# Performance work log

Hardware: AMD Instinct MI355X
Metric: run time of the kernel (lower is better)

## Reference

```python
import jax, jax.numpy as jnp
import numpy as np

H, W, C = 56, 56, 192
WS, SS = 7, 3          # window_size, shift_size
NH, HD = 6, 32         # num_heads, head_dim
N = WS * WS            # tokens per window = 49
HIDDEN = 4 * C
EPS = 1e-5


def _rel_pos_index():
    coords = np.stack(np.meshgrid(np.arange(WS), np.arange(WS), indexing='ij'))  # (2,ws,ws)
    flat = coords.reshape(2, -1)
    rel = flat[:, :, None] - flat[:, None, :]            # (2,N,N)
    rel = rel.transpose(1, 2, 0)
    rel[:, :, 0] += WS - 1
    rel[:, :, 1] += WS - 1
    rel[:, :, 0] *= 2 * WS - 1
    return rel.sum(-1)                                   # (N,N) int


def _attn_mask():
    img = np.zeros((H, W))
    cnt = 0
    for hs in (slice(0, -WS), slice(-WS, -SS), slice(-SS, None)):
        for ws_ in (slice(0, -WS), slice(-WS, -SS), slice(-SS, None)):
            img[hs, ws_] = cnt
            cnt += 1
    mw = img.reshape(H // WS, WS, W // WS, WS).transpose(0, 2, 1, 3).reshape(-1, N)  # (nW,N)
    diff = mw[:, None, :] - mw[:, :, None]
    return np.where(diff != 0, -100.0, 0.0).astype(np.float32)  # (nW,N,N)


REL_IDX = jnp.asarray(_rel_pos_index())
ATTN_MASK = jnp.asarray(_attn_mask())


def _ln(x, w, b):
    mu = x.mean(-1, keepdims=True)
    var = ((x - mu) ** 2).mean(-1, keepdims=True)
    return (x - mu) * jax.lax.rsqrt(var + EPS) * w + b


def _window_partition(x):
    # (B,H,W,C) -> (B*nW, N, C)
    B = x.shape[0]
    x = x.reshape(B, H // WS, WS, W // WS, WS, C)
    x = x.transpose(0, 1, 3, 2, 4, 5)
    return x.reshape(-1, N, C)


def _window_reverse(win, B):
    # (B*nW, N, C) -> (B,H,W,C)
    x = win.reshape(B, H // WS, W // WS, WS, WS, C)
    x = x.transpose(0, 1, 3, 2, 4, 5)
    return x.reshape(B, H, W, C)


def setup_inputs() -> dict:
    key = jax.random.key(0)
    ks = jax.random.split(key, 16)
    s = 0.02
    return {
        'x': jax.random.normal(ks[0], (64, H * W, C), jnp.float32),
        'norm1_w': jnp.ones((C,), jnp.float32),
        'norm1_b': jnp.zeros((C,), jnp.float32),
        'qkv_w': jax.random.normal(ks[1], (C, 3 * C), jnp.float32) * s,
        'qkv_b': jnp.zeros((3 * C,), jnp.float32),
        'rpb': jax.random.normal(ks[2], ((2 * WS - 1) ** 2, NH), jnp.float32) * s,
        'proj_w': jax.random.normal(ks[3], (C, C), jnp.float32) * s,
        'proj_b': jnp.zeros((C,), jnp.float32),
        'norm2_w': jnp.ones((C,), jnp.float32),
        'norm2_b': jnp.zeros((C,), jnp.float32),
        'fc1_w': jax.random.normal(ks[4], (C, HIDDEN), jnp.float32) * s,
        'fc1_b': jnp.zeros((HIDDEN,), jnp.float32),
        'fc2_w': jax.random.normal(ks[5], (HIDDEN, C), jnp.float32) * s,
        'fc2_b': jnp.zeros((C,), jnp.float32),
    }


def reference(x, norm1_w, norm1_b, qkv_w, qkv_b, rpb, proj_w, proj_b,
              norm2_w, norm2_b, fc1_w, fc1_b, fc2_w, fc2_b):
    B = x.shape[0]
    nW = (H // WS) * (W // WS)
    shortcut = x
    h = _ln(x, norm1_w, norm1_b).reshape(B, H, W, C)
    # cyclic shift
    h = jnp.roll(h, shift=(-SS, -SS), axis=(1, 2))
    xw = _window_partition(h)                                   # (B*nW, N, C)
    # windowed MHA
    qkv = (xw @ qkv_w + qkv_b).reshape(-1, N, 3, NH, HD).transpose(2, 0, 3, 1, 4)
    q, k, v = qkv[0], qkv[1], qkv[2]                            # (Bn, NH, N, HD)
    scale = HD ** -0.5
    attn = jnp.einsum('bhnd,bhmd->bhnm', q * scale, k)          # (Bn, NH, N, N)
    bias = rpb[REL_IDX.reshape(-1)].reshape(N, N, NH).transpose(2, 0, 1)
    attn = attn + bias[None]
    attn = attn.reshape(B, nW, NH, N, N) + ATTN_MASK[None, :, None]
    attn = jax.nn.softmax(attn.reshape(-1, NH, N, N), axis=-1)
    out = jnp.einsum('bhnm,bhmd->bhnd', attn, v)
    out = out.transpose(0, 2, 1, 3).reshape(-1, N, C)
    out = out @ proj_w + proj_b
    # reverse windows + un-shift
    h = _window_reverse(out, B)
    h = jnp.roll(h, shift=(SS, SS), axis=(1, 2)).reshape(B, H * W, C)
    x = shortcut + h
    # MLP (exact GELU, as torch nn.GELU default)
    m = _ln(x, norm2_w, norm2_b)
    m = jax.nn.gelu(m @ fc1_w + fc1_b, approximate=False)
    m = m @ fc2_w + fc2_b
    return x + m
```

## Files before the change

kernel.cpp:

```cpp
#include <hip/hip_runtime.h>
#include <hip/hip_bf16.h>

typedef __hip_bfloat16 bf16;
typedef __attribute__((ext_vector_type(8))) short short8;
typedef __attribute__((ext_vector_type(4))) float floatx4;

__device__ __forceinline__ floatx4 mfma16(short8 a, short8 b, floatx4 c) {
  return __builtin_amdgcn_mfma_f32_16x16x32_bf16(a, b, c, 0, 0, 0);
}

__device__ __forceinline__ float wave_sum(float v) {
#pragma unroll
  for (int off = 1; off < 64; off <<= 1) v += __shfl_xor(v, off);
  return v;
}

__device__ __forceinline__ void gload16(const void* g, void* l) {
  __builtin_amdgcn_global_load_lds(
      (const __attribute__((address_space(1))) unsigned int*)g,
      (__attribute__((address_space(3))) unsigned int*)l, 16, 0, 0);
}

__device__ __forceinline__ short8 lds_frag(const char* base, int row, int kb) {
  return *(const short8*)(base + row * 384 + (kb ^ ((row & 7) << 4)));
}
__device__ __forceinline__ short8 lds_frag128(const char* base, int row, int kb) {
  return *(const short8*)(base + row * 128 + (kb ^ ((row & 7) << 4)));
}

__global__ __launch_bounds__(256) void k_wt(const float* __restrict__ w,
                                            bf16* __restrict__ wt, int K, int N) {
  int id = blockIdx.x * 256 + threadIdx.x;
  if (id < K * N) {
    int n = id / K;
    int k = id - n * K;
    wt[id] = __float2bfloat16(w[(long)k * N + n]);
  }
}

template <bool GATHER>
__global__ __launch_bounds__(256) void k_ln(const float* __restrict__ xin,
                                            const float* __restrict__ w,
                                            const float* __restrict__ b,
                                            bf16* __restrict__ out) {
  const int lane = threadIdx.x & 63;
  const long row = (long)blockIdx.x * 4 + (threadIdx.x >> 6);
  long srow;
  if (GATHER) {
    int win = (int)(row / 49);
    int token = (int)(row - (long)win * 49);
    int bimg = win >> 6, wi = (win & 63) >> 3, wj = win & 7;
    int ti = token / 7, tj = token - ti * 7;
    int h = wi * 7 + ti + 3; if (h >= 56) h -= 56;
    int ww = wj * 7 + tj + 3; if (ww >= 56) ww -= 56;
    srow = (long)bimg * 3136 + h * 56 + ww;
  } else {
    srow = row;
  }
  const float* src = xin + srow * 192;
  float v0 = src[lane], v1 = src[lane + 64], v2 = src[lane + 128];
  float mu = wave_sum(v0 + v1 + v2) * (1.f / 192.f);
  float d0 = v0 - mu, d1 = v1 - mu, d2 = v2 - mu;
  float var = wave_sum(d0 * d0 + d1 * d1 + d2 * d2) * (1.f / 192.f);
  float rs = rsqrtf(var + 1e-5f);
  bf16* dst = out + row * 192;
  dst[lane]       = __float2bfloat16(d0 * rs * w[lane] + b[lane]);
  dst[lane + 64]  = __float2bfloat16(d1 * rs * w[lane + 64] + b[lane + 64]);
  dst[lane + 128] = __float2bfloat16(d2 * rs * w[lane + 128] + b[lane + 128]);
}

template <int EPI>
__global__ __launch_bounds__(256, 3) void k_gemm(const bf16* __restrict__ A,
                                                 const bf16* __restrict__ Bt,
                                                 const float* __restrict__ bias,
                                                 bf16* __restrict__ Cbf,
                                                 float* __restrict__ Cfp,
                                                 const float* __restrict__ res,
                                                 int Ncols, int K, long row0) {
  __shared__ __align__(16) char As[64 * 384];
  __shared__ __align__(16) char Bs[64 * 384];
  const int t = threadIdx.x;
  const int lane = t & 63, wid = t >> 6;
  const int lanelo = lane & 15, quad = lane >> 4;
  const long m0 = (long)blockIdx.x * 64;
  const int n0 = blockIdx.y * 64;
  const int wm = (wid >> 1) * 32, wn = (wid & 1) * 32;

  floatx4 acc[2][2];
#pragma unroll
  for (int i = 0; i < 2; i++)
#pragma unroll
    for (int j = 0; j < 2; j++) acc[i][j] = (floatx4){0.f, 0.f, 0.f, 0.f};

  const char* Ab = (const char*)(A + m0 * (long)K);
  const char* Bb = (const char*)(Bt + (long)n0 * K);
  const int ldab = 2 * K;

  for (int k0b = 0; k0b < 2 * K; k0b += 384) {
    __syncthreads();
#pragma unroll
    for (int i = 0; i < 6; i++) {
      int c = i * 256 + t;
      int r = c / 24;
      int j = c - r * 24;
      int be = (j * 16) ^ ((r & 7) << 4);
      gload16(Ab + (long)r * ldab + k0b + be, As + c * 16);
      gload16(Bb + (long)r * ldab + k0b + be, Bs + c * 16);
    }
    __syncthreads();

#pragma unroll
    for (int kk = 0; kk < 6; kk++) {
      const int kb = kk * 64 + quad * 16;
      short8 a0 = lds_frag(As, wm + lanelo, kb);
      short8 a1 = lds_frag(As, wm + 16 + lanelo, kb);
      short8 b0 = lds_frag(Bs, wn + lanelo, kb);
      short8 b1 = lds_frag(Bs, wn + 16 + lanelo, kb);
      acc[0][0] = mfma16(a0, b0, acc[0][0]);
      acc[0][1] = mfma16(a0, b1, acc[0][1]);
      acc[1][0] = mfma16(a1, b0, acc[1][0]);
      acc[1][1] = mfma16(a1, b1, acc[1][1]);
    }
  }

#pragma unroll
  for (int mi = 0; mi < 2; mi++) {
#pragma unroll
    for (int reg = 0; reg < 4; reg++) {
      const long r = m0 + wm + mi * 16 + quad * 4 + reg;
      long orow = r;
      if (EPI == 2) {
        const long rg = row0 + r;
        int win = (int)(rg / 49);
        int token = (int)(rg - (long)win * 49);
        int bimg = win >> 6, wi = (win & 63) >> 3, wj = win & 7;
        int ti = token / 7, tj = token - ti * 7;
        int h = wi * 7 + ti + 3; if (h >= 56) h -= 56;
        int ww = wj * 7 + tj + 3; if (ww >= 56) ww -= 56;
        orow = (long)bimg * 3136 + h * 56 + ww;
      }
#pragma unroll
      for (int ni = 0; ni < 2; ni++) {
        const int c = n0 + wn + ni * 16 + lanelo;
        float v = acc[mi][ni][reg] + bias[c];
        if (EPI == 0) {
          Cbf[r * Ncols + c] = __float2bfloat16(v);
        } else if (EPI == 1) {
          v = 0.5f * v * (1.f + erff(v * 0.70710678118654752f));
          Cbf[r * Ncols + c] = __float2bfloat16(v);
        } else if (EPI == 2) {
          Cfp[orow * 192 + c] = v + res[orow * 192 + c];
        } else {
          Cfp[r * 192 + c] = v + res[r * 192 + c];
        }
      }
    }
  }
}

__global__ __launch_bounds__(256, 3) void k_mlp(float* xres,
                                                const float* __restrict__ lw,
                                                const float* __restrict__ lb,
                                                const bf16* __restrict__ w1t,
                                                const float* __restrict__ b1,
                                                const bf16* __restrict__ w2t,
                                                const float* __restrict__ b2) {
  __shared__ __align__(16) char As[64 * 384];
  __shared__ __align__(16) char Hs[2][64 * 128];
  const int t = threadIdx.x, lane = t & 63, wid = t >> 6;
  const int lanelo = lane & 15, quad = lane >> 4;
  const long row0 = (long)blockIdx.x * 64;

  for (int i = 0; i < 16; i++) {
    int r = wid * 16 + i;
    const float* src = xres + (row0 + r) * 192;
    float v0 = src[lane], v1 = src[lane + 64], v2 = src[lane + 128];
    float mu = wave_sum(v0 + v1 + v2) * (1.f / 192.f);
    float d0 = v0 - mu, d1 = v1 - mu, d2 = v2 - mu;
    float var = wave_sum(d0 * d0 + d1 * d1 + d2 * d2) * (1.f / 192.f);
    float rs = rsqrtf(var + 1e-5f);
    int sw = (r & 7) << 4;
    *(bf16*)(As + r * 384 + ((2 * lane) ^ sw)) =
        __float2bfloat16(d0 * rs * lw[lane] + lb[lane]);
    *(bf16*)(As + r * 384 + ((128 + 2 * lane) ^ sw)) =
        __float2bfloat16(d1 * rs * lw[lane + 64] + lb[lane + 64]);
    *(bf16*)(As + r * 384 + ((256 + 2 * lane) ^ sw)) =
        __float2bfloat16(d2 * rs * lw[lane + 128] + lb[lane + 128]);
  }

  floatx4 acc2[4][3];
#pragma unroll
  for (int mi = 0; mi < 4; mi++)
#pragma unroll
    for (int ni = 0; ni < 3; ni++) acc2[mi][ni] = (floatx4){0.f, 0.f, 0.f, 0.f};

  __syncthreads();

  const int hcol = wid * 16 + lanelo;
  const int ocol0 = wid * 48;

  for (int nc = 0; nc < 12; nc++) {
    const char* w1p = (const char*)w1t + (long)(nc * 64 + hcol) * 384;
    floatx4 acc1[4];
#pragma unroll
    for (int mi = 0; mi < 4; mi++) acc1[mi] = (floatx4){0.f, 0.f, 0.f, 0.f};
#pragma unroll
    for (int kk = 0; kk < 6; kk++) {
      const int kb = kk * 64 + quad * 16;
      short8 bf = *(const short8*)(w1p + kb);
#pragma unroll
      for (int mi = 0; mi < 4; mi++) {
        short8 af = lds_frag(As, mi * 16 + lanelo, kb);
        acc1[mi] = mfma16(af, bf, acc1[mi]);
      }
    }

    char* H = Hs[nc & 1];
    const float b1v = b1[nc * 64 + hcol];
#pragma unroll
    for (int mi = 0; mi < 4; mi++)
#pragma unroll
      for (int reg = 0; reg < 4; reg++) {
        int r = mi * 16 + quad * 4 + reg;
        float v = acc1[mi][reg] + b1v;
        v = 0.5f * v * (1.f + erff(v * 0.70710678118654752f));
        *(bf16*)(H + r * 128 + ((2 * hcol) ^ ((r & 7) << 4))) =
            __float2bfloat16(v);
      }
    __syncthreads();

#pragma unroll
    for (int ks = 0; ks < 2; ks++) {
      const int kb = ks * 64 + quad * 16;
      short8 ha[4];
#pragma unroll
      for (int mi = 0; mi < 4; mi++)
        ha[mi] = lds_frag128(H, mi * 16 + lanelo, kb);
#pragma unroll
      for (int ni = 0; ni < 3; ni++) {
        short8 bv = *(const short8*)((const char*)w2t +
                                     (long)(ocol0 + ni * 16 + lanelo) * 1536 +
                                     nc * 128 + kb);
#pragma unroll
        for (int mi = 0; mi < 4; mi++)
          acc2[mi][ni] = mfma16(ha[mi], bv, acc2[mi][ni]);
      }
    }
  }

#pragma unroll
  for (int mi = 0; mi < 4; mi++)
#pragma unroll
    for (int ni = 0; ni < 3; ni++) {
      const int c = ocol0 + ni * 16 + lanelo;
      const float b2v = b2[c];
#pragma unroll
      for (int reg = 0; reg < 4; reg++) {
        const long g = (row0 + mi * 16 + quad * 4 + reg) * 192 + c;
        xres[g] = acc2[mi][ni][reg] + b2v + xres[g];
      }
    }
}

__global__ __launch_bounds__(256, 2) void k_attn(const bf16* __restrict__ qkv,
                                                 const float* __restrict__ rpb,
                                                 bf16* __restrict__ out) {
  __shared__ __align__(16) bf16 smem[4 * 7424];
  const int t = threadIdx.x, lane = t & 63, wid = t >> 6;
  const int lanelo = lane & 15, quad = lane >> 4;
  const int unit = blockIdx.x * 4 + wid;
  const int win = unit / 6, head = unit - win * 6;
  bf16* Qs = smem + wid * 7424;
  bf16* Ks = Qs + 2560;
  bf16* Vt = Qs + 5120;
  bf16* Ps = Qs;
  const long rowbase = (long)win * 49;
  const bf16* base = qkv + rowbase * 576 + head * 32;

  for (int idx = lane; idx < 196; idx += 64) {
    int tok = idx >> 2, ch = (idx & 3) * 8;
    *(uint4*)(&Qs[tok * 40 + ch]) = *(const uint4*)(base + (long)tok * 576 + ch);
    *(uint4*)(&Ks[tok * 40 + ch]) = *(const uint4*)(base + (long)tok * 576 + 192 + ch);
    union { uint4 u; bf16 h[8]; } tv;
    tv.u = *(const uint4*)(base + (long)tok * 576 + 384 + ch);
#pragma unroll
    for (int jj = 0; jj < 8; jj++) Vt[(ch + jj) * 72 + tok] = tv.h[jj];
  }
  for (int idx = lane; idx < 480; idx += 64) {
    int d = idx / 15, c = 49 + (idx - d * 15);
    Vt[d * 72 + c] = __float2bfloat16(0.f);
  }
  __syncthreads();

  floatx4 aS[4][4];
#pragma unroll
  for (int mi = 0; mi < 4; mi++)
#pragma unroll
    for (int ni = 0; ni < 4; ni++) aS[mi][ni] = (floatx4){0.f, 0.f, 0.f, 0.f};
  {
    short8 aq[4], bk[4];
#pragma unroll
    for (int mi = 0; mi < 4; mi++)
      aq[mi] = *(const short8*)(&Qs[(mi * 16 + lanelo) * 40 + quad * 8]);
#pragma unroll
    for (int ni = 0; ni < 4; ni++)
      bk[ni] = *(const short8*)(&Ks[(ni * 16 + lanelo) * 40 + quad * 8]);
#pragma unroll
    for (int mi = 0; mi < 4; mi++)
#pragma unroll
      for (int ni = 0; ni < 4; ni++) aS[mi][ni] = mfma16(aq[mi], bk[ni], aS[mi][ni]);
  }

  const int w_in = win & 63, wiw = w_in >> 3, wjw = w_in & 7;
  int cTi[4], cTj[4], cLab[4];
  bool cval[4];
#pragma unroll
  for (int ni = 0; ni < 4; ni++) {
    int j = ni * 16 + lanelo;
    cval[ni] = (j < 49);
    if (j > 48) j = 48;
    int ti = j / 7, tj = j - ti * 7;
    int rr = wiw * 7 + ti, cc = wjw * 7 + tj;
    cTi[ni] = ti;
    cTj[ni] = tj;
    cLab[ni] = ((rr < 49) ? 0 : (rr < 53 ? 1 : 2)) * 3 +
               ((cc < 49) ? 0 : (cc < 53 ? 1 : 2));
  }

  const float scale = 0.17677669529663687f;
  float rinv[16];
#pragma unroll
  for (int mi = 0; mi < 4; mi++) {
#pragma unroll
    for (int reg = 0; reg < 4; reg++) {
      int i = mi * 16 + quad * 4 + reg;
      if (i > 48) i = 48;
      int ti = i / 7, tj = i - ti * 7;
      int rr = wiw * 7 + ti, cc = wjw * 7 + tj;
      int rlab = ((rr < 49) ? 0 : (rr < 53 ? 1 : 2)) * 3 +
                 ((cc < 49) ? 0 : (cc < 53 ? 1 : 2));
      float sv[4];
      float mx = -1e30f;
#pragma unroll
      for (int ni = 0; ni < 4; ni++) {
        float s;
        if (cval[ni]) {
          int ridx = (ti - cTi[ni] + 6) * 13 + (tj - cTj[ni] + 6);
          float bb = rpb[ridx * 6 + head];
          if (rlab != cLab[ni]) bb -= 100.f;
          s = aS[mi][ni][reg] * scale + bb;
        } else {
          s = -1e30f;
        }
        sv[ni] = s;
        mx = fmaxf(mx, s);
      }
      mx = fmaxf(mx, __shfl_xor(mx, 1));
      mx = fmaxf(mx, __shfl_xor(mx, 2));
      mx = fmaxf(mx, __shfl_xor(mx, 4));
      mx = fmaxf(mx, __shfl_xor(mx, 8));
      float sum = 0.f;
#pragma unroll
      for (int ni = 0; ni < 4; ni++) {
        float p = __expf(sv[ni] - mx);
        sv[ni] = p;
        sum += p;
      }
      sum += __shfl_xor(sum, 1);
      sum += __shfl_xor(sum, 2);
      sum += __shfl_xor(sum, 4);
      sum += __shfl_xor(sum, 8);
      rinv[mi * 4 + reg] = 1.f / sum;
#pragma unroll
      for (int ni = 0; ni < 4; ni++) aS[mi][ni][reg] = sv[ni];
    }
  }
  __syncthreads();

#pragma unroll
  for (int mi = 0; mi < 4; mi++)
#pragma unroll
    for (int ni = 0; ni < 4; ni++)
#pragma unroll
      for (int reg = 0; reg < 4; reg++) {
        int i = mi * 16 + quad * 4 + reg, j = ni * 16 + lanelo;
        Ps[i * 72 + j] = __float2bfloat16(aS[mi][ni][reg]);
      }
  __syncthreads();

  floatx4 aO[4][2];
#pragma unroll
  for (int mi = 0; mi < 4; mi++)
#pragma unroll
    for (int ni = 0; ni < 2; ni++) aO[mi][ni] = (floatx4){0.f, 0.f, 0.f, 0.f};
#pragma unroll
  for (int k0 = 0; k0 < 64; k0 += 32) {
    short8 ap[4], bv[2];
#pragma unroll
    for (int mi = 0; mi < 4; mi++)
      ap[mi] = *(const short8*)(&Ps[(mi * 16 + lanelo) * 72 + k0 + quad * 8]);
#pragma unroll
    for (int ni = 0; ni < 2; ni++)
      bv[ni] = *(const short8*)(&Vt[(ni * 16 + lanelo) * 72 + k0 + quad * 8]);
#pragma unroll
    for (int mi = 0; mi < 4; mi++)
#pragma unroll
      for (int ni = 0; ni < 2; ni++) aO[mi][ni] = mfma16(ap[mi], bv[ni], aO[mi][ni]);
  }

#pragma unroll
  for (int mi = 0; mi < 4; mi++)
#pragma unroll
    for (int reg = 0; reg < 4; reg++) {
      int i = mi * 16 + quad * 4 + reg;
      if (i < 49) {
        float rv = rinv[mi * 4 + reg];
#pragma unroll
        for (int ni = 0; ni < 2; ni++) {
          int d = ni * 16 + lanelo;
          out[(rowbase + i) * 192 + head * 32 + d] =
              __float2bfloat16(aO[mi][ni][reg] * rv);
        }
      }
    }
}

extern "C" void kernel_launch(void* const* d_in, const int* in_sizes, int n_in,
                              void* d_out, int out_size, void* d_ws, size_t ws_size,
                              hipStream_t stream) {
  const float* x     = (const float*)d_in[0];
  const float* n1w   = (const float*)d_in[1];
  const float* n1b   = (const float*)d_in[2];
  const float* qkvw  = (const float*)d_in[3];
  const float* qkvb  = (const float*)d_in[4];
  const float* rpb   = (const float*)d_in[5];
  const float* projw = (const float*)d_in[6];
  const float* projb = (const float*)d_in[7];
  const float* n2w   = (const float*)d_in[8];
  const float* n2b   = (const float*)d_in[9];
  const float* fc1w  = (const float*)d_in[10];
  const float* fc1b  = (const float*)d_in[11];
  const float* fc2w  = (const float*)d_in[12];
  const float* fc2b  = (const float*)d_in[13];
  float* outf = (float*)d_out;

  const long CR = 50176;
  const int  NCH = 4;

  char* ws = (char*)d_ws;
  bf16* xw      = (bf16*)(ws + 0);
  bf16* qkvC    = (bf16*)(ws + 77070336LL);
  bf16* attC    = (bf16*)(ws + 134873088LL);
  bf16* wt_qkv  = (bf16*)(ws + 154140672LL);
  bf16* wt_proj = (bf16*)(ws + 154140672LL + 221184LL);
  bf16* wt_fc1  = (bf16*)(ws + 154140672LL + 294912LL);
  bf16* wt_fc2  = (bf16*)(ws + 154140672LL + 589824LL);

  k_wt<<<dim3((192 * 576 + 255) / 256), 256, 0, stream>>>(qkvw, wt_qkv, 192, 576);
  k_wt<<<dim3((192 * 192 + 255) / 256), 256, 0, stream>>>(projw, wt_proj, 192, 192);
  k_wt<<<dim3((192 * 768 + 255) / 256), 256, 0, stream>>>(fc1w, wt_fc1, 192, 768);
  k_wt<<<dim3((768 * 192 + 255) / 256), 256, 0, stream>>>(fc2w, wt_fc2, 768, 192);

  k_ln<true><<<dim3(50176), 256, 0, stream>>>(x, n1w, n1b, xw);

  for (int c = 0; c < NCH; c++) {
    const long r0 = c * CR;
    k_gemm<0><<<dim3(784, 9), 256, 0, stream>>>(xw + r0 * 192, wt_qkv, qkvb,
                                                qkvC, nullptr, nullptr, 576, 192, 0);
    k_attn<<<dim3(1536), 256, 0, stream>>>(qkvC, rpb, attC);
    k_gemm<2><<<dim3(784, 3), 256, 0, stream>>>(attC, wt_proj, projb, nullptr,
                                                outf, x, 192, 192, r0);
  }

  k_mlp<<<dim3(3136), 256, 0, stream>>>(outf, n2w, n2b, wt_fc1, fc1b,
                                        wt_fc2, fc2b);
}
```

Baseline: 1.020 ms.

## Fuse QKV GEMM, window attention and projection into one per-window kernel

```diff
diff --git a/kernel.cpp b/kernel.cpp
--- a/kernel.cpp
+++ b/kernel.cpp
@@ -3,6 +3,7 @@
 
 typedef __hip_bfloat16 bf16;
 typedef __attribute__((ext_vector_type(8))) short short8;
+typedef __attribute__((ext_vector_type(4))) short short4v;
 typedef __attribute__((ext_vector_type(4))) float floatx4;
 
 __device__ __forceinline__ floatx4 mfma16(short8 a, short8 b, floatx4 c) {
@@ -13,12 +14,6 @@
 #pragma unroll
   for (int off = 1; off < 64; off <<= 1) v += __shfl_xor(v, off);
   return v;
-}
-
-__device__ __forceinline__ void gload16(const void* g, void* l) {
-  __builtin_amdgcn_global_load_lds(
-      (const __attribute__((address_space(1))) unsigned int*)g,
-      (__attribute__((address_space(3))) unsigned int*)l, 16, 0, 0);
 }
 
 __device__ __forceinline__ short8 lds_frag(const char* base, int row, int kb) {
@@ -69,96 +64,219 @@
   dst[lane + 128] = __float2bfloat16(d2 * rs * w[lane + 128] + b[lane + 128]);
 }
 
-template <int EPI>
-__global__ __launch_bounds__(256, 3) void k_gemm(const bf16* __restrict__ A,
-                                                 const bf16* __restrict__ Bt,
-                                                 const float* __restrict__ bias,
-                                                 bf16* __restrict__ Cbf,
-                                                 float* __restrict__ Cfp,
-                                                 const float* __restrict__ res,
-                                                 int Ncols, int K, long row0) {
+__global__ __launch_bounds__(256, 2) void k_swin(const bf16* __restrict__ xw,
+                                                 const bf16* __restrict__ wq,
+                                                 const float* __restrict__ qkvb,
+                                                 const float* __restrict__ rpb,
+                                                 const bf16* __restrict__ wp,
+                                                 const float* __restrict__ projb,
+                                                 const float* __restrict__ xres,
+                                                 float* __restrict__ outf) {
   __shared__ __align__(16) char As[64 * 384];
-  __shared__ __align__(16) char Bs[64 * 384];
-  const int t = threadIdx.x;
-  const int lane = t & 63, wid = t >> 6;
+  __shared__ __align__(16) char Os[64 * 384];
+  __shared__ __align__(16) bf16 Qs[64 * 40];
+  __shared__ __align__(16) bf16 Ks[64 * 40];
+  __shared__ __align__(16) bf16 Vt[32 * 72];
+  __shared__ __align__(16) bf16 Ps[64 * 72];
+  const int t = threadIdx.x, lane = t & 63, wid = t >> 6;
   const int lanelo = lane & 15, quad = lane >> 4;
-  const long m0 = (long)blockIdx.x * 64;
-  const int n0 = blockIdx.y * 64;
-  const int wm = (wid >> 1) * 32, wn = (wid & 1) * 32;
-
-  floatx4 acc[2][2];
-#pragma unroll
-  for (int i = 0; i < 2; i++)
-#pragma unroll
-    for (int j = 0; j < 2; j++) acc[i][j] = (floatx4){0.f, 0.f, 0.f, 0.f};
-
-  const char* Ab = (const char*)(A + m0 * (long)K);
-  const char* Bb = (const char*)(Bt + (long)n0 * K);
-  const int ldab = 2 * K;
-
-  for (int k0b = 0; k0b < 2 * K; k0b += 384) {
-    __syncthreads();
+  const int w = blockIdx.x;
+  const long rowbase = (long)w * 49;
+  const int wm = wid * 16;
+
+  {
+    const char* src = (const char*)(xw + rowbase * 192);
 #pragma unroll
     for (int i = 0; i < 6; i++) {
       int c = i * 256 + t;
-      int r = c / 24;
-      int j = c - r * 24;
-      int be = (j * 16) ^ ((r & 7) << 4);
-      gload16(Ab + (long)r * ldab + k0b + be, As + c * 16);
-      gload16(Bb + (long)r * ldab + k0b + be, Bs + c * 16);
-    }
-    __syncthreads();
-
+      int r = c / 24, j = c - r * 24;
+      uint4 v;
+      if (r < 49) v = *(const uint4*)(src + (long)r * 384 + j * 16);
+      else { v.x = 0u; v.y = 0u; v.z = 0u; v.w = 0u; }
+      *(uint4*)(As + r * 384 + ((j * 16) ^ ((r & 7) << 4))) = v;
+    }
+  }
+
+  const int w_in = w & 63, wiw = w_in >> 3, wjw = w_in & 7;
+  int cTi[4], cTj[4], cLab[4];
+  bool cval[4];
+#pragma unroll
+  for (int ni = 0; ni < 4; ni++) {
+    int j = ni * 16 + lanelo;
+    cval[ni] = (j < 49);
+    if (j > 48) j = 48;
+    int ti = j / 7, tj = j - ti * 7;
+    int rr = wiw * 7 + ti, cc = wjw * 7 + tj;
+    cTi[ni] = ti; cTj[ni] = tj;
+    cLab[ni] = ((rr < 49) ? 0 : (rr < 53 ? 1 : 2)) * 3 +
+               ((cc < 49) ? 0 : (cc < 53 ? 1 : 2));
+  }
+  int ridx6[4][4];
+  float msub[4][4];
+#pragma unroll
+  for (int reg = 0; reg < 4; reg++) {
+    int i = wm + quad * 4 + reg;
+    if (i > 48) i = 48;
+    int ti = i / 7, tj = i - ti * 7;
+    int rr = wiw * 7 + ti, cc = wjw * 7 + tj;
+    int rlab = ((rr < 49) ? 0 : (rr < 53 ? 1 : 2)) * 3 +
+               ((cc < 49) ? 0 : (cc < 53 ? 1 : 2));
+#pragma unroll
+    for (int ni = 0; ni < 4; ni++) {
+      ridx6[reg][ni] = ((ti - cTi[ni] + 6) * 13 + (tj - cTj[ni] + 6)) * 6;
+      msub[reg][ni] = (rlab != cLab[ni]) ? 100.f : 0.f;
+    }
+  }
+  __syncthreads();
+
+  const float scale = 0.17677669529663687f;
+
+  for (int h = 0; h < 6; h++) {
+    floatx4 aq[6];
+#pragma unroll
+    for (int ni = 0; ni < 6; ni++) aq[ni] = (floatx4){0.f, 0.f, 0.f, 0.f};
 #pragma unroll
     for (int kk = 0; kk < 6; kk++) {
       const int kb = kk * 64 + quad * 16;
-      short8 a0 = lds_frag(As, wm + lanelo, kb);
-      short8 a1 = lds_frag(As, wm + 16 + lanelo, kb);
-      short8 b0 = lds_frag(Bs, wn + lanelo, kb);
-      short8 b1 = lds_frag(Bs, wn + 16 + lanelo, kb);
-      acc[0][0] = mfma16(a0, b0, acc[0][0]);
-      acc[0][1] = mfma16(a0, b1, acc[0][1]);
-      acc[1][0] = mfma16(a1, b0, acc[1][0]);
-      acc[1][1] = mfma16(a1, b1, acc[1][1]);
-    }
-  }
-
-#pragma unroll
-  for (int mi = 0; mi < 2; mi++) {
+      short8 af = lds_frag(As, wm + lanelo, kb);
+#pragma unroll
+      for (int ni = 0; ni < 6; ni++) {
+        const int wrow = (ni >> 1) * 192 + h * 32 + (ni & 1) * 16 + lanelo;
+        short8 bf = *(const short8*)((const char*)wq + (long)wrow * 384 + kb);
+        aq[ni] = mfma16(af, bf, aq[ni]);
+      }
+    }
+    __syncthreads();
+
+#pragma unroll
+    for (int ni = 0; ni < 6; ni++) {
+      const int p = ni >> 1;
+      const int d = (ni & 1) * 16 + lanelo;
+      const float bb = qkvb[p * 192 + h * 32 + d];
+      if (p < 2) {
+        bf16* dst = (p == 0) ? Qs : Ks;
+#pragma unroll
+        for (int reg = 0; reg < 4; reg++) {
+          int tok = wm + quad * 4 + reg;
+          dst[tok * 40 + d] = __float2bfloat16(aq[ni][reg] + bb);
+        }
+      } else {
+        union { short4v s; bf16 hh[4]; } pv;
+#pragma unroll
+        for (int reg = 0; reg < 4; reg++)
+          pv.hh[reg] = __float2bfloat16(aq[ni][reg] + bb);
+        *(short4v*)(&Vt[d * 72 + wm + quad * 4]) = pv.s;
+      }
+    }
+    __syncthreads();
+
+    short8 aqf = *(const short8*)(&Qs[(wm + lanelo) * 40 + quad * 8]);
+    floatx4 aS[4];
+#pragma unroll
+    for (int ni = 0; ni < 4; ni++) {
+      short8 bk = *(const short8*)(&Ks[(ni * 16 + lanelo) * 40 + quad * 8]);
+      aS[ni] = mfma16(aqf, bk, (floatx4){0.f, 0.f, 0.f, 0.f});
+    }
+
+    float rinv[4];
 #pragma unroll
     for (int reg = 0; reg < 4; reg++) {
-      const long r = m0 + wm + mi * 16 + quad * 4 + reg;
-      long orow = r;
-      if (EPI == 2) {
-        const long rg = row0 + r;
-        int win = (int)(rg / 49);
-        int token = (int)(rg - (long)win * 49);
-        int bimg = win >> 6, wi = (win & 63) >> 3, wj = win & 7;
-        int ti = token / 7, tj = token - ti * 7;
-        int h = wi * 7 + ti + 3; if (h >= 56) h -= 56;
-        int ww = wj * 7 + tj + 3; if (ww >= 56) ww -= 56;
-        orow = (long)bimg * 3136 + h * 56 + ww;
-      }
+      float sv[4];
+      float mx = -1e30f;
+#pragma unroll
+      for (int ni = 0; ni < 4; ni++) {
+        float s;
+        if (cval[ni]) {
+          s = aS[ni][reg] * scale + rpb[ridx6[reg][ni] + h] - msub[reg][ni];
+        } else {
+          s = -1e30f;
+        }
+        sv[ni] = s;
+        mx = fmaxf(mx, s);
+      }
+      mx = fmaxf(mx, __shfl_xor(mx, 1));
+      mx = fmaxf(mx, __shfl_xor(mx, 2));
+      mx = fmaxf(mx, __shfl_xor(mx, 4));
+      mx = fmaxf(mx, __shfl_xor(mx, 8));
+      float sum = 0.f;
+#pragma unroll
+      for (int ni = 0; ni < 4; ni++) {
+        float p = __expf(sv[ni] - mx);
+        sv[ni] = p;
+        sum += p;
+      }
+      sum += __shfl_xor(sum, 1);
+      sum += __shfl_xor(sum, 2);
+      sum += __shfl_xor(sum, 4);
+      sum += __shfl_xor(sum, 8);
+      rinv[reg] = 1.f / sum;
+#pragma unroll
+      for (int ni = 0; ni < 4; ni++) aS[ni][reg] = sv[ni];
+    }
+
+#pragma unroll
+    for (int ni = 0; ni < 4; ni++)
+#pragma unroll
+      for (int reg = 0; reg < 4; reg++)
+        Ps[(wm + quad * 4 + reg) * 72 + ni * 16 + lanelo] =
+            __float2bfloat16(aS[ni][reg]);
+
+    floatx4 aO[2];
+    aO[0] = (floatx4){0.f, 0.f, 0.f, 0.f};
+    aO[1] = (floatx4){0.f, 0.f, 0.f, 0.f};
+#pragma unroll
+    for (int ks = 0; ks < 2; ks++) {
+      short8 ap = *(const short8*)(&Ps[(wm + lanelo) * 72 + ks * 32 + quad * 8]);
 #pragma unroll
       for (int ni = 0; ni < 2; ni++) {
-        const int c = n0 + wn + ni * 16 + lanelo;
-        float v = acc[mi][ni][reg] + bias[c];
-        if (EPI == 0) {
-          Cbf[r * Ncols + c] = __float2bfloat16(v);
-        } else if (EPI == 1) {
-          v = 0.5f * v * (1.f + erff(v * 0.70710678118654752f));
-          Cbf[r * Ncols + c] = __float2bfloat16(v);
-        } else if (EPI == 2) {
-          Cfp[orow * 192 + c] = v + res[orow * 192 + c];
-        } else {
-          Cfp[r * 192 + c] = v + res[r * 192 + c];
-        }
-      }
-    }
-  }
-}
-
-__global__ __launch_bounds__(256, 3) void k_mlp(float* xres,
+        short8 bv = *(const short8*)(&Vt[(ni * 16 + lanelo) * 72 + ks * 32 + quad * 8]);
+        aO[ni] = mfma16(ap, bv, aO[ni]);
+      }
+    }
+#pragma unroll
+    for (int ni = 0; ni < 2; ni++)
+#pragma unroll
+      for (int reg = 0; reg < 4; reg++) {
+        int tok = wm + quad * 4 + reg;
+        int cb = 2 * (h * 32 + ni * 16 + lanelo);
+        *(bf16*)(Os + tok * 384 + (cb ^ ((tok & 7) << 4))) =
+            __float2bfloat16(aO[ni][reg] * rinv[reg]);
+      }
+  }
+  __syncthreads();
+
+  floatx4 accp[12];
+#pragma unroll
+  for (int ni = 0; ni < 12; ni++) accp[ni] = (floatx4){0.f, 0.f, 0.f, 0.f};
+#pragma unroll
+  for (int kk = 0; kk < 6; kk++) {
+    const int kb = kk * 64 + quad * 16;
+    short8 af = lds_frag(Os, wm + lanelo, kb);
+#pragma unroll
+    for (int ni = 0; ni < 12; ni++) {
+      short8 bf = *(const short8*)((const char*)wp +
+                                   (long)(ni * 16 + lanelo) * 384 + kb);
+      accp[ni] = mfma16(af, bf, accp[ni]);
+    }
+  }
+#pragma unroll
+  for (int reg = 0; reg < 4; reg++) {
+    const int tok = wm + quad * 4 + reg;
+    if (tok < 49) {
+      int ti = tok / 7, tj = tok - ti * 7;
+      int hh = wiw * 7 + ti + 3; if (hh >= 56) hh -= 56;
+      int ww2 = wjw * 7 + tj + 3; if (ww2 >= 56) ww2 -= 56;
+      const long orow = (long)(w >> 6) * 3136 + hh * 56 + ww2;
+#pragma unroll
+      for (int ni = 0; ni < 12; ni++) {
+        const int c = ni * 16 + lanelo;
+        outf[orow * 192 + c] = accp[ni][reg] + projb[c] + xres[orow * 192 + c];
+      }
+    }
+  }
+}
+
+__global__ __launch_bounds__(256, 4) void k_mlp(float* xres,
                                                 const float* __restrict__ lw,
                                                 const float* __restrict__ lb,
                                                 const bf16* __restrict__ w1t,
@@ -258,169 +376,6 @@
       for (int reg = 0; reg < 4; reg++) {
         const long g = (row0 + mi * 16 + quad * 4 + reg) * 192 + c;
         xres[g] = acc2[mi][ni][reg] + b2v + xres[g];
-      }
-    }
-}
-
-__global__ __launch_bounds__(256, 2) void k_attn(const bf16* __restrict__ qkv,
-                                                 const float* __restrict__ rpb,
-                                                 bf16* __restrict__ out) {
-  __shared__ __align__(16) bf16 smem[4 * 7424];
-  const int t = threadIdx.x, lane = t & 63, wid = t >> 6;
-  const int lanelo = lane & 15, quad = lane >> 4;
-  const int unit = blockIdx.x * 4 + wid;
-  const int win = unit / 6, head = unit - win * 6;
-  bf16* Qs = smem + wid * 7424;
-  bf16* Ks = Qs + 2560;
-  bf16* Vt = Qs + 5120;
-  bf16* Ps = Qs;
-  const long rowbase = (long)win * 49;
-  const bf16* base = qkv + rowbase * 576 + head * 32;
-
-  for (int idx = lane; idx < 196; idx += 64) {
-    int tok = idx >> 2, ch = (idx & 3) * 8;
-    *(uint4*)(&Qs[tok * 40 + ch]) = *(const uint4*)(base + (long)tok * 576 + ch);
-    *(uint4*)(&Ks[tok * 40 + ch]) = *(const uint4*)(base + (long)tok * 576 + 192 + ch);
-    union { uint4 u; bf16 h[8]; } tv;
-    tv.u = *(const uint4*)(base + (long)tok * 576 + 384 + ch);
-#pragma unroll
-    for (int jj = 0; jj < 8; jj++) Vt[(ch + jj) * 72 + tok] = tv.h[jj];
-  }
-  for (int idx = lane; idx < 480; idx += 64) {
-    int d = idx / 15, c = 49 + (idx - d * 15);
-    Vt[d * 72 + c] = __float2bfloat16(0.f);
-  }
-  __syncthreads();
-
-  floatx4 aS[4][4];
-#pragma unroll
-  for (int mi = 0; mi < 4; mi++)
-#pragma unroll
-    for (int ni = 0; ni < 4; ni++) aS[mi][ni] = (floatx4){0.f, 0.f, 0.f, 0.f};
-  {
-    short8 aq[4], bk[4];
-#pragma unroll
-    for (int mi = 0; mi < 4; mi++)
-      aq[mi] = *(const short8*)(&Qs[(mi * 16 + lanelo) * 40 + quad * 8]);
-#pragma unroll
-    for (int ni = 0; ni < 4; ni++)
-      bk[ni] = *(const short8*)(&Ks[(ni * 16 + lanelo) * 40 + quad * 8]);
-#pragma unroll
-    for (int mi = 0; mi < 4; mi++)
-#pragma unroll
-      for (int ni = 0; ni < 4; ni++) aS[mi][ni] = mfma16(aq[mi], bk[ni], aS[mi][ni]);
-  }
-
-  const int w_in = win & 63, wiw = w_in >> 3, wjw = w_in & 7;
-  int cTi[4], cTj[4], cLab[4];
-  bool cval[4];
-#pragma unroll
-  for (int ni = 0; ni < 4; ni++) {
-    int j = ni * 16 + lanelo;
-    cval[ni] = (j < 49);
-    if (j > 48) j = 48;
-    int ti = j / 7, tj = j - ti * 7;
-    int rr = wiw * 7 + ti, cc = wjw * 7 + tj;
-    cTi[ni] = ti;
-    cTj[ni] = tj;
-    cLab[ni] = ((rr < 49) ? 0 : (rr < 53 ? 1 : 2)) * 3 +
-               ((cc < 49) ? 0 : (cc < 53 ? 1 : 2));
-  }
-
-  const float scale = 0.17677669529663687f;
-  float rinv[16];
-#pragma unroll
-  for (int mi = 0; mi < 4; mi++) {
-#pragma unroll
-    for (int reg = 0; reg < 4; reg++) {
-      int i = mi * 16 + quad * 4 + reg;
-      if (i > 48) i = 48;
-      int ti = i / 7, tj = i - ti * 7;
-      int rr = wiw * 7 + ti, cc = wjw * 7 + tj;
-      int rlab = ((rr < 49) ? 0 : (rr < 53 ? 1 : 2)) * 3 +
-                 ((cc < 49) ? 0 : (cc < 53 ? 1 : 2));
-      float sv[4];
-      float mx = -1e30f;
-#pragma unroll
-      for (int ni = 0; ni < 4; ni++) {
-        float s;
-        if (cval[ni]) {
-          int ridx = (ti - cTi[ni] + 6) * 13 + (tj - cTj[ni] + 6);
-          float bb = rpb[ridx * 6 + head];
-          if (rlab != cLab[ni]) bb -= 100.f;
-          s = aS[mi][ni][reg] * scale + bb;
-        } else {
-          s = -1e30f;
-        }
-        sv[ni] = s;
-        mx = fmaxf(mx, s);
-      }
-      mx = fmaxf(mx, __shfl_xor(mx, 1));
-      mx = fmaxf(mx, __shfl_xor(mx, 2));
-      mx = fmaxf(mx, __shfl_xor(mx, 4));
-      mx = fmaxf(mx, __shfl_xor(mx, 8));
-      float sum = 0.f;
-#pragma unroll
-      for (int ni = 0; ni < 4; ni++) {
-        float p = __expf(sv[ni] - mx);
-        sv[ni] = p;
-        sum += p;
-      }
-      sum += __shfl_xor(sum, 1);
-      sum += __shfl_xor(sum, 2);
-      sum += __shfl_xor(sum, 4);
-      sum += __shfl_xor(sum, 8);
-      rinv[mi * 4 + reg] = 1.f / sum;
-#pragma unroll
-      for (int ni = 0; ni < 4; ni++) aS[mi][ni][reg] = sv[ni];
-    }
-  }
-  __syncthreads();
-
-#pragma unroll
-  for (int mi = 0; mi < 4; mi++)
-#pragma unroll
-    for (int ni = 0; ni < 4; ni++)
-#pragma unroll
-      for (int reg = 0; reg < 4; reg++) {
-        int i = mi * 16 + quad * 4 + reg, j = ni * 16 + lanelo;
-        Ps[i * 72 + j] = __float2bfloat16(aS[mi][ni][reg]);
-      }
-  __syncthreads();
-
-  floatx4 aO[4][2];
-#pragma unroll
-  for (int mi = 0; mi < 4; mi++)
-#pragma unroll
-    for (int ni = 0; ni < 2; ni++) aO[mi][ni] = (floatx4){0.f, 0.f, 0.f, 0.f};
-#pragma unroll
-  for (int k0 = 0; k0 < 64; k0 += 32) {
-    short8 ap[4], bv[2];
-#pragma unroll
-    for (int mi = 0; mi < 4; mi++)
-      ap[mi] = *(const short8*)(&Ps[(mi * 16 + lanelo) * 72 + k0 + quad * 8]);
-#pragma unroll
-    for (int ni = 0; ni < 2; ni++)
-      bv[ni] = *(const short8*)(&Vt[(ni * 16 + lanelo) * 72 + k0 + quad * 8]);
-#pragma unroll
-    for (int mi = 0; mi < 4; mi++)
-#pragma unroll
-      for (int ni = 0; ni < 2; ni++) aO[mi][ni] = mfma16(ap[mi], bv[ni], aO[mi][ni]);
-  }
-
-#pragma unroll
-  for (int mi = 0; mi < 4; mi++)
-#pragma unroll
-    for (int reg = 0; reg < 4; reg++) {
-      int i = mi * 16 + quad * 4 + reg;
-      if (i < 49) {
-        float rv = rinv[mi * 4 + reg];
-#pragma unroll
-        for (int ni = 0; ni < 2; ni++) {
-          int d = ni * 16 + lanelo;
-          out[(rowbase + i) * 192 + head * 32 + d] =
-              __float2bfloat16(aO[mi][ni][reg] * rv);
-        }
       }
     }
 }
@@ -444,13 +399,8 @@
   const float* fc2b  = (const float*)d_in[13];
   float* outf = (float*)d_out;
 
-  const long CR = 50176;
-  const int  NCH = 4;
-
   char* ws = (char*)d_ws;
   bf16* xw      = (bf16*)(ws + 0);
-  bf16* qkvC    = (bf16*)(ws + 77070336LL);
-  bf16* attC    = (bf16*)(ws + 134873088LL);
   bf16* wt_qkv  = (bf16*)(ws + 154140672LL);
   bf16* wt_proj = (bf16*)(ws + 154140672LL + 221184LL);
   bf16* wt_fc1  = (bf16*)(ws + 154140672LL + 294912LL);
@@ -463,14 +413,8 @@
 
   k_ln<true><<<dim3(50176), 256, 0, stream>>>(x, n1w, n1b, xw);
 
-  for (int c = 0; c < NCH; c++) {
-    const long r0 = c * CR;
-    k_gemm<0><<<dim3(784, 9), 256, 0, stream>>>(xw + r0 * 192, wt_qkv, qkvb,
-                                                qkvC, nullptr, nullptr, 576, 192, 0);
-    k_attn<<<dim3(1536), 256, 0, stream>>>(qkvC, rpb, attC);
-    k_gemm<2><<<dim3(784, 3), 256, 0, stream>>>(attC, wt_proj, projb, nullptr,
-                                                outf, x, 192, 192, r0);
-  }
+  k_swin<<<dim3(4096), 256, 0, stream>>>(xw, wt_qkv, qkvb, rpb, wt_proj, projb,
+                                         x, outf);
 
   k_mlp<<<dim3(3136), 256, 0, stream>>>(outf, n2w, n2b, wt_fc1, fc1b,
                                         wt_fc2, fc2b);
```

Measured after the change: 1.262 ms. 23.7% more time.

## Fuse QKV projection into windowed attention kernel and drop chunked launches

Applied to the files above, without the earlier changes.

```diff
diff --git a/kernel.cpp b/kernel.cpp
--- a/kernel.cpp
+++ b/kernel.cpp
@@ -3,6 +3,7 @@
 
 typedef __hip_bfloat16 bf16;
 typedef __attribute__((ext_vector_type(8))) short short8;
+typedef __attribute__((ext_vector_type(4))) short short4v;
 typedef __attribute__((ext_vector_type(4))) float floatx4;
 
 __device__ __forceinline__ floatx4 mfma16(short8 a, short8 b, floatx4 c) {
@@ -158,7 +159,192 @@
   }
 }
 
-__global__ __launch_bounds__(256, 3) void k_mlp(float* xres,
+__global__ __launch_bounds__(256, 2) void k_attn2(const bf16* __restrict__ xw,
+                                                  const bf16* __restrict__ wq,
+                                                  const float* __restrict__ qkvb,
+                                                  const float* __restrict__ rpb,
+                                                  bf16* __restrict__ attC) {
+  __shared__ __align__(16) bf16 smem[4 * 7424];
+  const int t = threadIdx.x, lane = t & 63, wid = t >> 6;
+  const int lanelo = lane & 15, quad = lane >> 4;
+  const int unit = blockIdx.x * 4 + wid;
+  const int win = unit / 6, head = unit - win * 6;
+  bf16* Qs = smem + wid * 7424;
+  bf16* Ks = Qs + 2560;
+  bf16* Vt = Qs + 5120;
+  bf16* Ps = Qs;
+  const long rowbase = (long)win * 49;
+
+  const int w_in = win & 63, wiw = w_in >> 3, wjw = w_in & 7;
+  int cTi[4], cTj[4], cLab[4];
+  bool cval[4];
+#pragma unroll
+  for (int ni = 0; ni < 4; ni++) {
+    int j = ni * 16 + lanelo;
+    cval[ni] = (j < 49);
+    if (j > 48) j = 48;
+    int ti = j / 7, tj = j - ti * 7;
+    int rr = wiw * 7 + ti, cc = wjw * 7 + tj;
+    cTi[ni] = ti; cTj[ni] = tj;
+    cLab[ni] = ((rr < 49) ? 0 : (rr < 53 ? 1 : 2)) * 3 +
+               ((cc < 49) ? 0 : (cc < 53 ? 1 : 2));
+  }
+
+  const float scale = 0.17677669529663687f;
+
+  {
+    floatx4 aq[4][6];
+#pragma unroll
+    for (int mi = 0; mi < 4; mi++)
+#pragma unroll
+      for (int ni = 0; ni < 6; ni++) aq[mi][ni] = (floatx4){0.f, 0.f, 0.f, 0.f};
+#pragma unroll
+    for (int kk = 0; kk < 6; kk++) {
+      const int kb = kk * 64 + quad * 16;
+      short8 af[4];
+#pragma unroll
+      for (int mi = 0; mi < 4; mi++)
+        af[mi] = *(const short8*)((const char*)xw +
+                                  (rowbase + mi * 16 + lanelo) * 384 + kb);
+#pragma unroll
+      for (int ni = 0; ni < 6; ni++) {
+        const int wrow = (ni >> 1) * 192 + head * 32 + (ni & 1) * 16 + lanelo;
+        short8 bf = *(const short8*)((const char*)wq + (long)wrow * 384 + kb);
+#pragma unroll
+        for (int mi = 0; mi < 4; mi++) aq[mi][ni] = mfma16(af[mi], bf, aq[mi][ni]);
+      }
+    }
+#pragma unroll
+    for (int ni = 0; ni < 6; ni++) {
+      const int p = ni >> 1;
+      const int d = (ni & 1) * 16 + lanelo;
+      const float bb = qkvb[p * 192 + head * 32 + d];
+      if (p < 2) {
+        bf16* dst = (p == 0) ? Qs : Ks;
+#pragma unroll
+        for (int mi = 0; mi < 4; mi++)
+#pragma unroll
+          for (int reg = 0; reg < 4; reg++) {
+            int tok = mi * 16 + quad * 4 + reg;
+            dst[tok * 40 + d] = __float2bfloat16(aq[mi][ni][reg] + bb);
+          }
+      } else {
+#pragma unroll
+        for (int mi = 0; mi < 4; mi++) {
+          union { short4v s; bf16 hh[4]; } pv;
+#pragma unroll
+          for (int reg = 0; reg < 4; reg++)
+            pv.hh[reg] = __float2bfloat16(aq[mi][ni][reg] + bb);
+          *(short4v*)(&Vt[d * 72 + mi * 16 + quad * 4]) = pv.s;
+        }
+      }
+    }
+  }
+
+  float rinv[16];
+  {
+    floatx4 aS[4][4];
+#pragma unroll
+    for (int mi = 0; mi < 4; mi++) {
+      short8 aqf = *(const short8*)(&Qs[(mi * 16 + lanelo) * 40 + quad * 8]);
+#pragma unroll
+      for (int ni = 0; ni < 4; ni++) {
+        short8 bk = *(const short8*)(&Ks[(ni * 16 + lanelo) * 40 + quad * 8]);
+        aS[mi][ni] = mfma16(aqf, bk, (floatx4){0.f, 0.f, 0.f, 0.f});
+      }
+    }
+#pragma unroll
+    for (int mi = 0; mi < 4; mi++) {
+#pragma unroll
+      for (int reg = 0; reg < 4; reg++) {
+        int i = mi * 16 + quad * 4 + reg;
+        if (i > 48) i = 48;
+        int ti = i / 7, tj = i - ti * 7;
+        int rr = wiw * 7 + ti, cc = wjw * 7 + tj;
+        int rlab = ((rr < 49) ? 0 : (rr < 53 ? 1 : 2)) * 3 +
+                   ((cc < 49) ? 0 : (cc < 53 ? 1 : 2));
+        float sv[4];
+        float mx = -1e30f;
+#pragma unroll
+        for (int ni = 0; ni < 4; ni++) {
+          float s;
+          if (cval[ni]) {
+            int ridx = (ti - cTi[ni] + 6) * 13 + (tj - cTj[ni] + 6);
+            float bb = rpb[ridx * 6 + head];
+            if (rlab != cLab[ni]) bb -= 100.f;
+            s = aS[mi][ni][reg] * scale + bb;
+          } else {
+            s = -1e30f;
+          }
+          sv[ni] = s;
+          mx = fmaxf(mx, s);
+        }
+        mx = fmaxf(mx, __shfl_xor(mx, 1));
+        mx = fmaxf(mx, __shfl_xor(mx, 2));
+        mx = fmaxf(mx, __shfl_xor(mx, 4));
+        mx = fmaxf(mx, __shfl_xor(mx, 8));
+        float sum = 0.f;
+#pragma unroll
+        for (int ni = 0; ni < 4; ni++) {
+          float p = __expf(sv[ni] - mx);
+          sv[ni] = p;
+          sum += p;
+        }
+        sum += __shfl_xor(sum, 1);
+        sum += __shfl_xor(sum, 2);
+        sum += __shfl_xor(sum, 4);
+        sum += __shfl_xor(sum, 8);
+        rinv[mi * 4 + reg] = 1.f / sum;
+#pragma unroll
+        for (int ni = 0; ni < 4; ni++) aS[mi][ni][reg] = sv[ni];
+      }
+    }
+#pragma unroll
+    for (int mi = 0; mi < 4; mi++)
+#pragma unroll
+      for (int ni = 0; ni < 4; ni++)
+#pragma unroll
+        for (int reg = 0; reg < 4; reg++)
+          Ps[(mi * 16 + quad * 4 + reg) * 72 + ni * 16 + lanelo] =
+              __float2bfloat16(aS[mi][ni][reg]);
+  }
+
+  floatx4 aO[4][2];
+#pragma unroll
+  for (int mi = 0; mi < 4; mi++)
+#pragma unroll
+    for (int ni = 0; ni < 2; ni++) aO[mi][ni] = (floatx4){0.f, 0.f, 0.f, 0.f};
+#pragma unroll
+  for (int ks = 0; ks < 2; ks++) {
+#pragma unroll
+    for (int mi = 0; mi < 4; mi++) {
+      short8 ap = *(const short8*)(&Ps[(mi * 16 + lanelo) * 72 + ks * 32 + quad * 8]);
+#pragma unroll
+      for (int ni = 0; ni < 2; ni++) {
+        short8 bv = *(const short8*)(&Vt[(ni * 16 + lanelo) * 72 + ks * 32 + quad * 8]);
+        aO[mi][ni] = mfma16(ap, bv, aO[mi][ni]);
+      }
+    }
+  }
+
+#pragma unroll
+  for (int mi = 0; mi < 4; mi++)
+#pragma unroll
+    for (int reg = 0; reg < 4; reg++) {
+      int i = mi * 16 + quad * 4 + reg;
+      if (i < 49) {
+        float rv = rinv[mi * 4 + reg];
+#pragma unroll
+        for (int ni = 0; ni < 2; ni++) {
+          int d = ni * 16 + lanelo;
+          attC[(rowbase + i) * 192 + head * 32 + d] =
+              __float2bfloat16(aO[mi][ni][reg] * rv);
+        }
+      }
+    }
+}
+
+__global__ __launch_bounds__(256, 4) void k_mlp(float* xres,
                                                 const float* __restrict__ lw,
                                                 const float* __restrict__ lb,
                                                 const bf16* __restrict__ w1t,
@@ -258,169 +444,6 @@
       for (int reg = 0; reg < 4; reg++) {
         const long g = (row0 + mi * 16 + quad * 4 + reg) * 192 + c;
         xres[g] = acc2[mi][ni][reg] + b2v + xres[g];
-      }
-    }
-}
-
-__global__ __launch_bounds__(256, 2) void k_attn(const bf16* __restrict__ qkv,
-                                                 const float* __restrict__ rpb,
-                                                 bf16* __restrict__ out) {
-  __shared__ __align__(16) bf16 smem[4 * 7424];
-  const int t = threadIdx.x, lane = t & 63, wid = t >> 6;
-  const int lanelo = lane & 15, quad = lane >> 4;
-  const int unit = blockIdx.x * 4 + wid;
-  const int win = unit / 6, head = unit - win * 6;
-  bf16* Qs = smem + wid * 7424;
-  bf16* Ks = Qs + 2560;
-  bf16* Vt = Qs + 5120;
-  bf16* Ps = Qs;
-  const long rowbase = (long)win * 49;
-  const bf16* base = qkv + rowbase * 576 + head * 32;
-
-  for (int idx = lane; idx < 196; idx += 64) {
-    int tok = idx >> 2, ch = (idx & 3) * 8;
-    *(uint4*)(&Qs[tok * 40 + ch]) = *(const uint4*)(base + (long)tok * 576 + ch);
-    *(uint4*)(&Ks[tok * 40 + ch]) = *(const uint4*)(base + (long)tok * 576 + 192 + ch);
-    union { uint4 u; bf16 h[8]; } tv;
-    tv.u = *(const uint4*)(base + (long)tok * 576 + 384 + ch);
-#pragma unroll
-    for (int jj = 0; jj < 8; jj++) Vt[(ch + jj) * 72 + tok] = tv.h[jj];
-  }
-  for (int idx = lane; idx < 480; idx += 64) {
-    int d = idx / 15, c = 49 + (idx - d * 15);
-    Vt[d * 72 + c] = __float2bfloat16(0.f);
-  }
-  __syncthreads();
-
-  floatx4 aS[4][4];
-#pragma unroll
-  for (int mi = 0; mi < 4; mi++)
-#pragma unroll
-    for (int ni = 0; ni < 4; ni++) aS[mi][ni] = (floatx4){0.f, 0.f, 0.f, 0.f};
-  {
-    short8 aq[4], bk[4];
-#pragma unroll
-    for (int mi = 0; mi < 4; mi++)
-      aq[mi] = *(const short8*)(&Qs[(mi * 16 + lanelo) * 40 + quad * 8]);
-#pragma unroll
-    for (int ni = 0; ni < 4; ni++)
-      bk[ni] = *(const short8*)(&Ks[(ni * 16 + lanelo) * 40 + quad * 8]);
-#pragma unroll
-    for (int mi = 0; mi < 4; mi++)
-#pragma unroll
-      for (int ni = 0; ni < 4; ni++) aS[mi][ni] = mfma16(aq[mi], bk[ni], aS[mi][ni]);
-  }
-
-  const int w_in = win & 63, wiw = w_in >> 3, wjw = w_in & 7;
-  int cTi[4], cTj[4], cLab[4];
-  bool cval[4];
-#pragma unroll
-  for (int ni = 0; ni < 4; ni++) {
-    int j = ni * 16 + lanelo;
-    cval[ni] = (j < 49);
-    if (j > 48) j = 48;
-    int ti = j / 7, tj = j - ti * 7;
-    int rr = wiw * 7 + ti, cc = wjw * 7 + tj;
-    cTi[ni] = ti;
-    cTj[ni] = tj;
-    cLab[ni] = ((rr < 49) ? 0 : (rr < 53 ? 1 : 2)) * 3 +
-               ((cc < 49) ? 0 : (cc < 53 ? 1 : 2));
-  }
-
-  const float scale = 0.17677669529663687f;
-  float rinv[16];
-#pragma unroll
-  for (int mi = 0; mi < 4; mi++) {
-#pragma unroll
-    for (int reg = 0; reg < 4; reg++) {
-      int i = mi * 16 + quad * 4 + reg;
-      if (i > 48) i = 48;
-      int ti = i / 7, tj = i - ti * 7;
-      int rr = wiw * 7 + ti, cc = wjw * 7 + tj;
-      int rlab = ((rr < 49) ? 0 : (rr < 53 ? 1 : 2)) * 3 +
-                 ((cc < 49) ? 0 : (cc < 53 ? 1 : 2));
-      float sv[4];
-      float mx = -1e30f;
-#pragma unroll
-      for (int ni = 0; ni < 4; ni++) {
-        float s;
-        if (cval[ni]) {
-          int ridx = (ti - cTi[ni] + 6) * 13 + (tj - cTj[ni] + 6);
-          float bb = rpb[ridx * 6 + head];
-          if (rlab != cLab[ni]) bb -= 100.f;
-          s = aS[mi][ni][reg] * scale + bb;
-        } else {
-          s = -1e30f;
-        }
-        sv[ni] = s;
-        mx = fmaxf(mx, s);
-      }
-      mx = fmaxf(mx, __shfl_xor(mx, 1));
-      mx = fmaxf(mx, __shfl_xor(mx, 2));
-      mx = fmaxf(mx, __shfl_xor(mx, 4));
-      mx = fmaxf(mx, __shfl_xor(mx, 8));
-      float sum = 0.f;
-#pragma unroll
-      for (int ni = 0; ni < 4; ni++) {
-        float p = __expf(sv[ni] - mx);
-        sv[ni] = p;
-        sum += p;
-      }
-      sum += __shfl_xor(sum, 1);
-      sum += __shfl_xor(sum, 2);
-      sum += __shfl_xor(sum, 4);
-      sum += __shfl_xor(sum, 8);
-      rinv[mi * 4 + reg] = 1.f / sum;
-#pragma unroll
-      for (int ni = 0; ni < 4; ni++) aS[mi][ni][reg] = sv[ni];
-    }
-  }
-  __syncthreads();
-
-#pragma unroll
-  for (int mi = 0; mi < 4; mi++)
-#pragma unroll
-    for (int ni = 0; ni < 4; ni++)
-#pragma unroll
-      for (int reg = 0; reg < 4; reg++) {
-        int i = mi * 16 + quad * 4 + reg, j = ni * 16 + lanelo;
-        Ps[i * 72 + j] = __float2bfloat16(aS[mi][ni][reg]);
-      }
-  __syncthreads();
-
-  floatx4 aO[4][2];
-#pragma unroll
-  for (int mi = 0; mi < 4; mi++)
-#pragma unroll
-    for (int ni = 0; ni < 2; ni++) aO[mi][ni] = (floatx4){0.f, 0.f, 0.f, 0.f};
-#pragma unroll
-  for (int k0 = 0; k0 < 64; k0 += 32) {
-    short8 ap[4], bv[2];
-#pragma unroll
-    for (int mi = 0; mi < 4; mi++)
-      ap[mi] = *(const short8*)(&Ps[(mi * 16 + lanelo) * 72 + k0 + quad * 8]);
-#pragma unroll
-    for (int ni = 0; ni < 2; ni++)
-      bv[ni] = *(const short8*)(&Vt[(ni * 16 + lanelo) * 72 + k0 + quad * 8]);
-#pragma unroll
-    for (int mi = 0; mi < 4; mi++)
-#pragma unroll
-      for (int ni = 0; ni < 2; ni++) aO[mi][ni] = mfma16(ap[mi], bv[ni], aO[mi][ni]);
-  }
-
-#pragma unroll
-  for (int mi = 0; mi < 4; mi++)
-#pragma unroll
-    for (int reg = 0; reg < 4; reg++) {
-      int i = mi * 16 + quad * 4 + reg;
-      if (i < 49) {
-        float rv = rinv[mi * 4 + reg];
-#pragma unroll
-        for (int ni = 0; ni < 2; ni++) {
-          int d = ni * 16 + lanelo;
-          out[(rowbase + i) * 192 + head * 32 + d] =
-              __float2bfloat16(aO[mi][ni][reg] * rv);
-        }
       }
     }
 }
@@ -444,13 +467,9 @@
   const float* fc2b  = (const float*)d_in[13];
   float* outf = (float*)d_out;
 
-  const long CR = 50176;
-  const int  NCH = 4;
-
   char* ws = (char*)d_ws;
   bf16* xw      = (bf16*)(ws + 0);
-  bf16* qkvC    = (bf16*)(ws + 77070336LL);
-  bf16* attC    = (bf16*)(ws + 134873088LL);
+  bf16* attC    = (bf16*)(ws + 77070336LL);
   bf16* wt_qkv  = (bf16*)(ws + 154140672LL);
   bf16* wt_proj = (bf16*)(ws + 154140672LL + 221184LL);
   bf16* wt_fc1  = (bf16*)(ws + 154140672LL + 294912LL);
@@ -463,14 +482,10 @@
 
   k_ln<true><<<dim3(50176), 256, 0, stream>>>(x, n1w, n1b, xw);
 
-  for (int c = 0; c < NCH; c++) {
-    const long r0 = c * CR;
-    k_gemm<0><<<dim3(784, 9), 256, 0, stream>>>(xw + r0 * 192, wt_qkv, qkvb,
-                                                qkvC, nullptr, nullptr, 576, 192, 0);
-    k_attn<<<dim3(1536), 256, 0, stream>>>(qkvC, rpb, attC);
-    k_gemm<2><<<dim3(784, 3), 256, 0, stream>>>(attC, wt_proj, projb, nullptr,
-                                                outf, x, 192, 192, r0);
-  }
+  k_attn2<<<dim3(6144), 256, 0, stream>>>(xw, wt_qkv, qkvb, rpb, attC);
+
+  k_gemm<2><<<dim3(3136, 3), 256, 0, stream>>>(attC, wt_proj, projb, nullptr,
+                                               outf, x, 192, 192, 0);
 
   k_mlp<<<dim3(3136), 256, 0, stream>>>(outf, n2w, n2b, wt_fc1, fc1b,
                                         wt_fc2, fc2b);
```

Result: faster. 993.1 us (-2.6%).
